# Kernel tuning notes

Measured on AMD Instinct MI355X. Metric: run time of the kernel, lower is better.

## Reference

```python
import jax, jax.numpy as jnp
import numpy as np

N = 8192      # total nodes
B = 8         # graphs in batch
L = 1024      # nodes per graph (max_len)
E = 262144    # edges (before self loops)
IN = 64       # in_channels
H = 8         # heads
C = 32        # hidden_channels (per-head out dim)
D = H * C     # 256, d_model
DFF = 2048    # transformer FFN dim (torch default)
NEG = -1e9


def setup_inputs() -> dict:
    key = jax.random.key(0)
    ks = jax.random.split(key, 24)
    def p(i, shape):
        return jax.random.normal(ks[i], shape, jnp.float32) * 0.02
    x = jax.random.normal(ks[0], (N, IN), jnp.float32)
    src = jax.random.randint(ks[1], (E,), 0, N)
    dst = (src // L) * L + jax.random.randint(ks[2], (E,), 0, L)  # keep edges within a graph
    edge_index = jnp.stack([src, dst]).astype(jnp.int32)
    batch = (jnp.arange(N) // L).astype(jnp.int32)
    return dict(
        x=x, edge_index=edge_index, batch=batch,
        gat_W0=p(3, (D, IN)), gat_W12=p(4, (2, D, D)),
        gat_att_src=p(5, (3, H, C)), gat_att_dst=p(6, (3, H, C)), gat_bias=p(7, (3, D)),
        tf_qkv_w=p(8, (2, 3 * D, D)), tf_qkv_b=p(9, (2, 3 * D)),
        tf_out_w=p(10, (2, D, D)), tf_out_b=p(11, (2, D)),
        tf_ln1_w=jnp.ones((2, D)), tf_ln1_b=jnp.zeros((2, D)),
        tf_ln2_w=jnp.ones((2, D)), tf_ln2_b=jnp.zeros((2, D)),
        tf_ff1_w=p(12, (2, DFF, D)), tf_ff1_b=p(13, (2, DFF)),
        tf_ff2_w=p(14, (2, D, DFF)), tf_ff2_b=p(15, (2, D)),
        pred_w=p(16, (3, D)), pred_b=p(17, (3,)),
    )


def _gat(x, src, dst, W, att_s, att_d, bias):
    # PyG GATConv, concat=True, add_self_loops (appended in caller), eval (no dropout)
    h = (x @ W.T).reshape(-1, H, C)                       # [N,H,C]
    a_s = (h * att_s).sum(-1)                             # [N,H]
    a_d = (h * att_d).sum(-1)
    e = jax.nn.leaky_relu(a_s[src] + a_d[dst], 0.2)       # [E+N,H]
    m = jax.ops.segment_max(e, dst, num_segments=N)       # per-dst softmax
    e = jnp.exp(e - m[dst])
    s = jax.ops.segment_sum(e, dst, num_segments=N)
    alpha = e / s[dst]
    out = jax.ops.segment_sum(h[src] * alpha[..., None], dst, num_segments=N)
    return out.reshape(-1, D) + bias


def _ln(x, w, b):
    mu = x.mean(-1, keepdims=True)
    v = ((x - mu) ** 2).mean(-1, keepdims=True)
    return (x - mu) / jnp.sqrt(v + 1e-5) * w + b


def _tf_layer(x, mask, qkv_w, qkv_b, out_w, out_b, ln1w, ln1b, ln2w, ln2b, f1w, f1b, f2w, f2b):
    # torch TransformerEncoderLayer (post-LN, relu), key padding mask, eval mode
    qkv = x @ qkv_w.T + qkv_b                              # [B,L,3D]
    q, k, v = jnp.split(qkv, 3, -1)
    sh = lambda t: t.reshape(B, L, H, D // H)
    q, k, v = sh(q), sh(k), sh(v)
    sc = jnp.einsum('bqhd,bkhd->bhqk', q, k) * (1.0 / float(np.sqrt(D // H)))
    sc = jnp.where(mask[:, None, None, :], NEG, sc)
    a = jax.nn.softmax(sc, -1)
    o = jnp.einsum('bhqk,bkhd->bqhd', a, v).reshape(B, L, D)
    x = _ln(x + o @ out_w.T + out_b, ln1w, ln1b)
    f = jax.nn.relu(x @ f1w.T + f1b) @ f2w.T + f2b
    return _ln(x + f, ln2w, ln2b)


def reference(x, edge_index, batch, gat_W0, gat_W12, gat_att_src, gat_att_dst, gat_bias,
              tf_qkv_w, tf_qkv_b, tf_out_w, tf_out_b, tf_ln1_w, tf_ln1_b, tf_ln2_w, tf_ln2_b,
              tf_ff1_w, tf_ff1_b, tf_ff2_w, tf_ff2_b, pred_w, pred_b):
    loops = jnp.arange(N, dtype=edge_index.dtype)
    src = jnp.concatenate([edge_index[0], loops])
    dst = jnp.concatenate([edge_index[1], loops])
    h = jax.nn.relu(_gat(x, src, dst, gat_W0, gat_att_src[0], gat_att_dst[0], gat_bias[0]))
    for i in range(2):
        h = jax.nn.relu(_gat(h, src, dst, gat_W12[i], gat_att_src[i + 1], gat_att_dst[i + 1], gat_bias[i + 1]))
    # ragged -> padded [B, L, D] (vectorized scatter instead of python loop)
    seq_lens = jax.ops.segment_sum(jnp.ones(N, jnp.int32), batch, num_segments=B)
    starts = jnp.cumsum(seq_lens) - seq_lens
    pos = jnp.arange(N) - starts[batch]
    xp = jnp.zeros((B, L, D), h.dtype).at[batch, pos].set(h)
    mask = jnp.arange(L)[None, :] >= seq_lens[:, None]     # True = padded key
    for i in range(2):
        xp = _tf_layer(xp, mask, tf_qkv_w[i], tf_qkv_b[i], tf_out_w[i], tf_out_b[i],
                       tf_ln1_w[i], tf_ln1_b[i], tf_ln2_w[i], tf_ln2_b[i],
                       tf_ff1_w[i], tf_ff1_b[i], tf_ff2_w[i], tf_ff2_b[i])
    return xp @ pred_w.T + pred_b                          # [B,L,3]
```

## Files before the change

kernel.cpp:

```cpp
#include <hip/hip_runtime.h>
#include <hip/hip_bf16.h>

#define NN 8192
#define EE 262144
#define BB 8
#define LL 1024
#define HH 8
#define DD 256
#define DFFN 2048

typedef short s8v __attribute__((ext_vector_type(8)));
typedef float f32x4 __attribute__((ext_vector_type(4)));
typedef unsigned short ushort;

__device__ inline ushort f2bf(float f) {
    unsigned u = __float_as_uint(f);
    u = (u + 0x7fffu + ((u >> 16) & 1u)) >> 16;
    return (ushort)u;
}
__device__ inline float bf2f(ushort u) {
    return __uint_as_float(((unsigned)u) << 16);
}

template<bool BIAS, bool RELU, bool RES, bool WF, bool WB>
__global__ __launch_bounds__(256) void mgemm_kernel(
    const ushort* __restrict__ A, const ushort* __restrict__ W,
    const float* __restrict__ bias, const float* __restrict__ res,
    float* __restrict__ Cf, ushort* __restrict__ Cb, int M, int N, int K)
{
    __shared__ ushort As[128 * 64];
    __shared__ ushort Bs[128 * 64];
    int t = threadIdx.x;
    int l = t & 63;
    int quad = l >> 4, l15 = l & 15;
    int r7 = l15 & 7;
    int w = t >> 6;
    int wm = (w >> 1) * 64, wn = (w & 1) * 64;
    int m0 = blockIdx.x * 128, n0 = blockIdx.y * 128;

    f32x4 z = {0.f, 0.f, 0.f, 0.f};
    f32x4 acc[4][4];
#pragma unroll
    for (int i = 0; i < 4; ++i)
#pragma unroll
        for (int j = 0; j < 4; ++j) acc[i][j] = z;

    for (int k0 = 0; k0 < K; k0 += 64) {
#pragma unroll
        for (int i = 0; i < 4; ++i) {
            int chunk = i * 256 + t;
            int r = chunk >> 3, p = chunk & 7;
            int qs = (p ^ (r & 7)) * 8;
            __builtin_amdgcn_global_load_lds(
                (const __attribute__((address_space(1))) unsigned int*)
                    (A + (size_t)(m0 + r) * K + k0 + qs),
                (__attribute__((address_space(3))) unsigned int*)(As + chunk * 8), 16, 0, 0);
            __builtin_amdgcn_global_load_lds(
                (const __attribute__((address_space(1))) unsigned int*)
                    (W + (size_t)(n0 + r) * K + k0 + qs),
                (__attribute__((address_space(3))) unsigned int*)(Bs + chunk * 8), 16, 0, 0);
        }
        __syncthreads();
#pragma unroll
        for (int kk = 0; kk < 2; ++kk) {
            int off = ((kk * 4 + quad) ^ r7) * 8;
            s8v af[4], bfv[4];
#pragma unroll
            for (int i = 0; i < 4; ++i) {
                af[i]  = *(const s8v*)(As + (wm + i * 16 + l15) * 64 + off);
                bfv[i] = *(const s8v*)(Bs + (wn + i * 16 + l15) * 64 + off);
            }
#pragma unroll
            for (int mi = 0; mi < 4; ++mi)
#pragma unroll
                for (int ni = 0; ni < 4; ++ni)
                    acc[mi][ni] = __builtin_amdgcn_mfma_f32_16x16x32_bf16(
                        af[mi], bfv[ni], acc[mi][ni], 0, 0, 0);
        }
        __syncthreads();
    }

#pragma unroll
    for (int mi = 0; mi < 4; ++mi) {
#pragma unroll
        for (int ni = 0; ni < 4; ++ni) {
            int n = n0 + wn + ni * 16 + l15;
#pragma unroll
            for (int r = 0; r < 4; ++r) {
                int m = m0 + wm + mi * 16 + quad * 4 + r;
                float v = acc[mi][ni][r];
                if (BIAS) v += bias[n];
                if (RES)  v += res[(size_t)m * N + n];
                if (RELU) v = fmaxf(v, 0.f);
                if (WF) Cf[(size_t)m * N + n] = v;
                if (WB) Cb[(size_t)m * N + n] = f2bf(v);
            }
        }
    }
}

template<bool BIAS, bool RELU, bool RES, bool WF, bool WB, bool ASD>
__global__ __launch_bounds__(256) void mgemm64_kernel(
    const ushort* __restrict__ A, const ushort* __restrict__ W,
    const float* __restrict__ bias, const float* __restrict__ res,
    float* __restrict__ Cf, ushort* __restrict__ Cb,
    const float* __restrict__ atts, const float* __restrict__ attd,
    float* __restrict__ a_s, float* __restrict__ a_d, int M, int N, int K)
{
    __shared__ ushort As[64 * 64];
    __shared__ ushort Bs[64 * 64];
    int t = threadIdx.x;
    int l = t & 63;
    int quad = l >> 4, l15 = l & 15;
    int r7 = l15 & 7;
    int w = t >> 6;
    int wm = (w >> 1) * 32, wn = (w & 1) * 32;
    int m0 = blockIdx.x * 64, n0 = blockIdx.y * 64;

    f32x4 z = {0.f, 0.f, 0.f, 0.f};
    f32x4 acc[2][2];
#pragma unroll
    for (int i = 0; i < 2; ++i)
#pragma unroll
        for (int j = 0; j < 2; ++j) acc[i][j] = z;

    for (int k0 = 0; k0 < K; k0 += 64) {
#pragma unroll
        for (int i = 0; i < 2; ++i) {
            int chunk = i * 256 + t;
            int r = chunk >> 3, p = chunk & 7;
            int qs = (p ^ (r & 7)) * 8;
            __builtin_amdgcn_global_load_lds(
                (const __attribute__((address_space(1))) unsigned int*)
                    (A + (size_t)(m0 + r) * K + k0 + qs),
                (__attribute__((address_space(3))) unsigned int*)(As + chunk * 8), 16, 0, 0);
            __builtin_amdgcn_global_load_lds(
                (const __attribute__((address_space(1))) unsigned int*)
                    (W + (size_t)(n0 + r) * K + k0 + qs),
                (__attribute__((address_space(3))) unsigned int*)(Bs + chunk * 8), 16, 0, 0);
        }
        __syncthreads();
#pragma unroll
        for (int kk = 0; kk < 2; ++kk) {
            s8v af[2], bfv[2];
            int off = ((kk * 4 + quad) ^ r7) * 8;
#pragma unroll
            for (int i = 0; i < 2; ++i) {
                af[i]  = *(const s8v*)(As + (wm + i * 16 + l15) * 64 + off);
                bfv[i] = *(const s8v*)(Bs + (wn + i * 16 + l15) * 64 + off);
            }
#pragma unroll
            for (int mi = 0; mi < 2; ++mi)
#pragma unroll
                for (int ni = 0; ni < 2; ++ni)
                    acc[mi][ni] = __builtin_amdgcn_mfma_f32_16x16x32_bf16(
                        af[mi], bfv[ni], acc[mi][ni], 0, 0, 0);
        }
        __syncthreads();
    }

#pragma unroll
    for (int mi = 0; mi < 2; ++mi) {
#pragma unroll
        for (int ni = 0; ni < 2; ++ni) {
            int n = n0 + wn + ni * 16 + l15;
#pragma unroll
            for (int r = 0; r < 4; ++r) {
                int m = m0 + wm + mi * 16 + quad * 4 + r;
                float v = acc[mi][ni][r];
                if (BIAS) v += bias[n];
                if (RES)  v += res[(size_t)m * N + n];
                if (RELU) v = fmaxf(v, 0.f);
                if (WF) Cf[(size_t)m * N + n] = v;
                if (WB) Cb[(size_t)m * N + n] = f2bf(v);
            }
        }
    }

    if (ASD) {
        int head = ((n0 + wn) >> 5) & 7;
        float as0 = atts[head * 32 + l15];
        float as1 = atts[head * 32 + 16 + l15];
        float ad0 = attd[head * 32 + l15];
        float ad1 = attd[head * 32 + 16 + l15];
#pragma unroll
        for (int mi = 0; mi < 2; ++mi)
#pragma unroll
            for (int r = 0; r < 4; ++r) {
                float sp = acc[mi][0][r] * as0 + acc[mi][1][r] * as1;
                float dp = acc[mi][0][r] * ad0 + acc[mi][1][r] * ad1;
#pragma unroll
                for (int off = 1; off < 16; off <<= 1) {
                    sp += __shfl_xor(sp, off);
                    dp += __shfl_xor(dp, off);
                }
                if (l15 == 0) {
                    int m = m0 + wm + mi * 16 + quad * 4 + r;
                    a_s[m * 8 + head] = sp;
                    a_d[m * 8 + head] = dp;
                }
            }
    }
}

__global__ __launch_bounds__(256) void mgemm_ln_kernel(
    const ushort* __restrict__ A, const ushort* __restrict__ W,
    const float* __restrict__ bias, const float* __restrict__ res,
    const float* __restrict__ lnw, const float* __restrict__ lnbb,
    float* __restrict__ Xf, ushort* __restrict__ Xb, int M, int K)
{
    __shared__ ushort As[16 * 64];
    __shared__ ushort Bs[256 * 64];
    __shared__ float red[2][4][16];

    int t = threadIdx.x;
    int l = t & 63;
    int quad = l >> 4, l15 = l & 15;
    int r7 = l15 & 7;
    int w = t >> 6;
    int m0 = blockIdx.x * 16;
    int n0w = w * 64;

    f32x4 z = {0.f, 0.f, 0.f, 0.f};
    f32x4 acc[4];
#pragma unroll
    for (int i = 0; i < 4; ++i) acc[i] = z;

    for (int k0 = 0; k0 < K; k0 += 64) {
#pragma unroll
        for (int i = 0; i < 8; ++i) {
            int chunk = i * 256 + t;
            int r = chunk >> 3, p = chunk & 7;
            int qs = (p ^ (r & 7)) * 8;
            __builtin_amdgcn_global_load_lds(
                (const __attribute__((address_space(1))) unsigned int*)
                    (W + (size_t)r * K + k0 + qs),
                (__attribute__((address_space(3))) unsigned int*)(Bs + chunk * 8), 16, 0, 0);
        }
        if (t < 128) {
            int r = t >> 3, p = t & 7;
            int qs = (p ^ (r & 7)) * 8;
            __builtin_amdgcn_global_load_lds(
                (const __attribute__((address_space(1))) unsigned int*)
                    (A + (size_t)(m0 + r) * K + k0 + qs),
                (__attribute__((address_space(3))) unsigned int*)(As + t * 8), 16, 0, 0);
        }
        __syncthreads();
#pragma unroll
        for (int kk = 0; kk < 2; ++kk) {
            int off = ((kk * 4 + quad) ^ r7) * 8;
            s8v af = *(const s8v*)(As + l15 * 64 + off);
#pragma unroll
            for (int ni = 0; ni < 4; ++ni) {
                s8v bfv = *(const s8v*)(Bs + (n0w + ni * 16 + l15) * 64 + off);
                acc[ni] = __builtin_amdgcn_mfma_f32_16x16x32_bf16(af, bfv, acc[ni], 0, 0, 0);
            }
        }
        __syncthreads();
    }

    float v[4][4];
#pragma unroll
    for (int ni = 0; ni < 4; ++ni) {
        int n = n0w + ni * 16 + l15;
        float bi = bias[n];
#pragma unroll
        for (int r = 0; r < 4; ++r) {
            int m = m0 + quad * 4 + r;
            v[ni][r] = acc[ni][r] + bi + res[(size_t)m * DD + n];
        }
    }
    float s1[4], s2[4];
#pragma unroll
    for (int r = 0; r < 4; ++r) {
        s1[r] = 0.f; s2[r] = 0.f;
#pragma unroll
        for (int ni = 0; ni < 4; ++ni) { s1[r] += v[ni][r]; s2[r] += v[ni][r] * v[ni][r]; }
#pragma unroll
        for (int off = 1; off < 16; off <<= 1) {
            s1[r] += __shfl_xor(s1[r], off);
            s2[r] += __shfl_xor(s2[r], off);
        }
    }
    if (l15 == 0)
#pragma unroll
        for (int r = 0; r < 4; ++r) {
            red[0][w][quad * 4 + r] = s1[r];
            red[1][w][quad * 4 + r] = s2[r];
        }
    __syncthreads();
    float mu[4], rstd[4];
#pragma unroll
    for (int r = 0; r < 4; ++r) {
        int row = quad * 4 + r;
        float S1 = red[0][0][row] + red[0][1][row] + red[0][2][row] + red[0][3][row];
        float S2 = red[1][0][row] + red[1][1][row] + red[1][2][row] + red[1][3][row];
        mu[r] = S1 * (1.f / 256.f);
        float var = S2 * (1.f / 256.f) - mu[r] * mu[r];
        rstd[r] = rsqrtf(fmaxf(var, 0.f) + 1e-5f);
    }
#pragma unroll
    for (int ni = 0; ni < 4; ++ni) {
        int n = n0w + ni * 16 + l15;
        float wl = lnw[n], bl = lnbb[n];
#pragma unroll
        for (int r = 0; r < 4; ++r) {
            int m = m0 + quad * 4 + r;
            float o = (v[ni][r] - mu[r]) * rstd[r] * wl + bl;
            Xf[(size_t)m * DD + n] = o;
            Xb[(size_t)m * DD + n] = f2bf(o);
        }
    }
}

__global__ __launch_bounds__(256) void mgemm_qkv_kernel(
    const ushort* __restrict__ A, const ushort* __restrict__ W,
    const float* __restrict__ bias,
    ushort* __restrict__ Qb, ushort* __restrict__ Kb, ushort* __restrict__ Vt,
    int M, int K)
{
    __shared__ ushort As[64 * 64];
    __shared__ ushort Bs[64 * 64];
    int t = threadIdx.x;
    int l = t & 63;
    int quad = l >> 4, l15 = l & 15;
    int r7 = l15 & 7;
    int w = t >> 6;
    int wm = (w >> 1) * 32, wn = (w & 1) * 32;
    int m0 = blockIdx.x * 64, n0 = blockIdx.y * 64;

    f32x4 z = {0.f, 0.f, 0.f, 0.f};
    f32x4 acc[2][2];
#pragma unroll
    for (int i = 0; i < 2; ++i)
#pragma unroll
        for (int j = 0; j < 2; ++j) acc[i][j] = z;

    for (int k0 = 0; k0 < K; k0 += 64) {
#pragma unroll
        for (int i = 0; i < 2; ++i) {
            int chunk = i * 256 + t;
            int r = chunk >> 3, p = chunk & 7;
            int qs = (p ^ (r & 7)) * 8;
            __builtin_amdgcn_global_load_lds(
                (const __attribute__((address_space(1))) unsigned int*)
                    (A + (size_t)(m0 + r) * K + k0 + qs),
                (__attribute__((address_space(3))) unsigned int*)(As + chunk * 8), 16, 0, 0);
            __builtin_amdgcn_global_load_lds(
                (const __attribute__((address_space(1))) unsigned int*)
                    (W + (size_t)(n0 + r) * K + k0 + qs),
                (__attribute__((address_space(3))) unsigned int*)(Bs + chunk * 8), 16, 0, 0);
        }
        __syncthreads();
#pragma unroll
        for (int kk = 0; kk < 2; ++kk) {
            s8v af[2], bfv[2];
            int off = ((kk * 4 + quad) ^ r7) * 8;
#pragma unroll
            for (int i = 0; i < 2; ++i) {
                af[i]  = *(const s8v*)(As + (wm + i * 16 + l15) * 64 + off);
                bfv[i] = *(const s8v*)(Bs + (wn + i * 16 + l15) * 64 + off);
            }
#pragma unroll
            for (int mi = 0; mi < 2; ++mi)
#pragma unroll
                for (int ni = 0; ni < 2; ++ni)
                    acc[mi][ni] = __builtin_amdgcn_mfma_f32_16x16x32_bf16(
                        af[mi], bfv[ni], acc[mi][ni], 0, 0, 0);
        }
        __syncthreads();
    }

#pragma unroll
    for (int mi = 0; mi < 2; ++mi) {
#pragma unroll
        for (int ni = 0; ni < 2; ++ni) {
            int n = n0 + wn + ni * 16 + l15;
            int sec = n >> 8, hc = n & 255;
            int hh = hc >> 5, c = hc & 31;
            float bv = bias[n];
#pragma unroll
            for (int r = 0; r < 4; ++r) {
                int m = m0 + wm + mi * 16 + quad * 4 + r;
                float v = acc[mi][ni][r] + bv;
                int b = m >> 10, ll2 = m & 1023;
                int bh = b * 8 + hh;
                if (sec == 0)
                    Qb[(size_t)bh * 32768 + ll2 * 32 + c] = f2bf(v * 0.17677669529663687f);
                else if (sec == 1)
                    Kb[(size_t)bh * 32768 + ll2 * 32 + c] = f2bf(v);
                else
                    Vt[(size_t)bh * 32768 + c * 1024 + ll2] = f2bf(v);
            }
        }
    }
}

__global__ __launch_bounds__(256) void castall_kernel(
    const float* __restrict__ W0, const float* __restrict__ W12,
    const float* __restrict__ qkvw, const float* __restrict__ outw,
    const float* __restrict__ f1w, const float* __restrict__ f2w,
    const float* __restrict__ x,
    ushort* __restrict__ W0b, ushort* __restrict__ W12b,
    ushort* __restrict__ qkvb, ushort* __restrict__ outb,
    ushort* __restrict__ f1b, ushort* __restrict__ f2b,
    ushort* __restrict__ xb, int* __restrict__ deg)
{
    int tid = blockIdx.x * 256 + threadIdx.x;
    if (tid < 2048) *(int4*)(deg + tid * 4) = make_int4(0, 0, 0, 0);
    int e = tid * 4;
    if (e >= 3293184) return;
    const float* s; ushort* d; int off;
    if (e < 16384)        { s = W0;   d = W0b;  off = e; }
    else if (e < 147456)  { s = W12;  d = W12b; off = e - 16384; }
    else if (e < 540672)  { s = qkvw; d = qkvb; off = e - 147456; }
    else if (e < 671744)  { s = outw; d = outb; off = e - 540672; }
    else if (e < 1720320) { s = f1w;  d = f1b;  off = e - 671744; }
    else if (e < 2768896) { s = f2w;  d = f2b;  off = e - 1720320; }
    else                  { s = x;    d = xb;   off = e - 2768896; }
    float4 v = *(const float4*)(s + off);
    d[off + 0] = f2bf(v.x); d[off + 1] = f2bf(v.y);
    d[off + 2] = f2bf(v.z); d[off + 3] = f2bf(v.w);
}

__global__ void scatter_kernel(const int* __restrict__ ei, int* __restrict__ deg,
                               int* __restrict__ col)
{
    int e = blockIdx.x * 256 + threadIdx.x;
    if (e >= EE + NN) return;
    int s, d;
    if (e < EE) { s = ei[e]; d = ei[EE + e]; } else { s = e - EE; d = s; }
    int slot = atomicAdd(&deg[d], 1);
    col[(d << 7) + slot] = s;
}

__global__ __launch_bounds__(256) void gat_agg_kernel(
    const ushort* __restrict__ hlinb, const float* __restrict__ a_s,
    const float* __restrict__ a_d, const int* __restrict__ deg,
    const int* __restrict__ col, const float* __restrict__ bias,
    float* __restrict__ alpha_e,
    float* __restrict__ out, ushort* __restrict__ outb)
{
    int wid = threadIdx.x >> 6, lane = threadIdx.x & 63;
    int dst = blockIdx.x * 4 + wid;
    int start = dst << 7;
    int end = start + deg[dst];
    float ad[HH];
#pragma unroll
    for (int h = 0; h < HH; ++h) ad[h] = a_d[(size_t)dst * HH + h];

    float sm[HH];
#pragma unroll
    for (int h = 0; h < HH; ++h) sm[h] = 0.f;
    for (int e = start + lane; e < end; e += 64) {
        int s = col[e];
        float* al = alpha_e + (size_t)e * HH;
#pragma unroll
        for (int h = 0; h < HH; ++h) {
            float v = a_s[(size_t)s * HH + h] + ad[h];
            v = v > 0.f ? v : 0.2f * v;
            float p = __expf(v);
            sm[h] += p;
            al[h] = p;
        }
    }
#pragma unroll
    for (int h = 0; h < HH; ++h)
#pragma unroll
        for (int off = 32; off; off >>= 1) sm[h] += __shfl_xor(sm[h], off);

    int myh = lane >> 3;
    float invs = 1.f / sm[myh];
    float a0 = 0.f, a1 = 0.f, a2 = 0.f, a3 = 0.f;
    int e = start;
    for (; e + 4 <= end; e += 4) {
        int s0 = col[e], s1 = col[e + 1], s2 = col[e + 2], s3 = col[e + 3];
        float al0 = alpha_e[(size_t)e * HH + myh] * invs;
        float al1 = alpha_e[(size_t)(e + 1) * HH + myh] * invs;
        float al2 = alpha_e[(size_t)(e + 2) * HH + myh] * invs;
        float al3 = alpha_e[(size_t)(e + 3) * HH + myh] * invs;
        uint2 h0 = *(const uint2*)(hlinb + (size_t)s0 * DD + lane * 4);
        uint2 h1 = *(const uint2*)(hlinb + (size_t)s1 * DD + lane * 4);
        uint2 h2 = *(const uint2*)(hlinb + (size_t)s2 * DD + lane * 4);
        uint2 h3 = *(const uint2*)(hlinb + (size_t)s3 * DD + lane * 4);
        a0 += al0 * bf2f((ushort)(h0.x & 0xffff)) + al1 * bf2f((ushort)(h1.x & 0xffff))
            + al2 * bf2f((ushort)(h2.x & 0xffff)) + al3 * bf2f((ushort)(h3.x & 0xffff));
        a1 += al0 * bf2f((ushort)(h0.x >> 16)) + al1 * bf2f((ushort)(h1.x >> 16))
            + al2 * bf2f((ushort)(h2.x >> 16)) + al3 * bf2f((ushort)(h3.x >> 16));
        a2 += al0 * bf2f((ushort)(h0.y & 0xffff)) + al1 * bf2f((ushort)(h1.y & 0xffff))
            + al2 * bf2f((ushort)(h2.y & 0xffff)) + al3 * bf2f((ushort)(h3.y & 0xffff));
        a3 += al0 * bf2f((ushort)(h0.y >> 16)) + al1 * bf2f((ushort)(h1.y >> 16))
            + al2 * bf2f((ushort)(h2.y >> 16)) + al3 * bf2f((ushort)(h3.y >> 16));
    }
    for (; e < end; ++e) {
        int s = col[e];
        float alpha = alpha_e[(size_t)e * HH + myh] * invs;
        uint2 hv = *(const uint2*)(hlinb + (size_t)s * DD + lane * 4);
        a0 += alpha * bf2f((ushort)(hv.x & 0xffff));
        a1 += alpha * bf2f((ushort)(hv.x >> 16));
        a2 += alpha * bf2f((ushort)(hv.y & 0xffff));
        a3 += alpha * bf2f((ushort)(hv.y >> 16));
    }
    float4 bv = *(const float4*)(bias + lane * 4);
    float r0 = fmaxf(a0 + bv.x, 0.f);
    float r1 = fmaxf(a1 + bv.y, 0.f);
    float r2 = fmaxf(a2 + bv.z, 0.f);
    float r3 = fmaxf(a3 + bv.w, 0.f);
    float* op = out + (size_t)dst * DD + lane * 4;
    op[0] = r0; op[1] = r1; op[2] = r2; op[3] = r3;
    ushort* ob = outb + (size_t)dst * DD + lane * 4;
    ob[0] = f2bf(r0); ob[1] = f2bf(r1); ob[2] = f2bf(r2); ob[3] = f2bf(r3);
}

__global__ __launch_bounds__(256, 2) void attn_flash_kernel(
    const ushort* __restrict__ Qb, const ushort* __restrict__ Kb,
    const ushort* __restrict__ Vt, ushort* __restrict__ outb)
{
    __shared__ ushort Ks[2][128 * 32];
    __shared__ ushort Vs[2][32 * 128];
    __shared__ ushort pw[4][32][132];

    int t = threadIdx.x;
    int w = t >> 6, lane = t & 63;
    int quad = lane >> 4, l15 = lane & 15;
    int kq = (quad ^ ((l15 >> 1) & 3)) * 8;
    int bh = blockIdx.y;
    int q0 = blockIdx.x * 128 + w * 32;
    int b = bh >> 3, h = bh & 7;

    const ushort* qbase = Qb + (size_t)bh * 32768;
    const ushort* kbase = Kb + (size_t)bh * 32768;
    const ushort* vbase = Vt + (size_t)bh * 32768;

    s8v aq0 = *(const s8v*)(qbase + (q0 + l15) * 32 + quad * 8);
    s8v aq1 = *(const s8v*)(qbase + (q0 + 16 + l15) * 32 + quad * 8);

    int i0 = t, i1 = 256 + t;
    int kr0 = i0 >> 2, kcs0 = (((i0 & 3)) ^ ((kr0 >> 1) & 3)) * 8;
    int kr1 = i1 >> 2, kcs1 = (((i1 & 3)) ^ ((kr1 >> 1) & 3)) * 8;
    int vr0 = i0 >> 4, vcs0 = ((i0 & 15) ^ (vr0 & 15)) * 8;
    int vr1 = i1 >> 4, vcs1 = ((i1 & 15) ^ (vr1 & 15)) * 8;

#define STAGE(ch, bf)                                                          \
    {                                                                          \
        int j0 = (ch) * 128;                                                   \
        __builtin_amdgcn_global_load_lds(                                      \
            (const __attribute__((address_space(1))) unsigned int*)            \
                (kbase + (size_t)(j0 + kr0) * 32 + kcs0),                      \
            (__attribute__((address_space(3))) unsigned int*)(Ks[bf] + i0 * 8), 16, 0, 0); \
        __builtin_amdgcn_global_load_lds(                                      \
            (const __attribute__((address_space(1))) unsigned int*)            \
                (kbase + (size_t)(j0 + kr1) * 32 + kcs1),                      \
            (__attribute__((address_space(3))) unsigned int*)(Ks[bf] + i1 * 8), 16, 0, 0); \
        __builtin_amdgcn_global_load_lds(                                      \
            (const __attribute__((address_space(1))) unsigned int*)            \
                (vbase + (size_t)vr0 * 1024 + j0 + vcs0),                      \
            (__attribute__((address_space(3))) unsigned int*)(Vs[bf] + i0 * 8), 16, 0, 0); \
        __builtin_amdgcn_global_load_lds(                                      \
            (const __attribute__((address_space(1))) unsigned int*)            \
                (vbase + (size_t)vr1 * 1024 + j0 + vcs1),                      \
            (__attribute__((address_space(3))) unsigned int*)(Vs[bf] + i1 * 8), 16, 0, 0); \
    }

    f32x4 z = {0.f, 0.f, 0.f, 0.f};
    f32x4 o00 = z, o01 = z, o10 = z, o11 = z;
    float lden0[4] = {0.f, 0.f, 0.f, 0.f};
    float lden1[4] = {0.f, 0.f, 0.f, 0.f};

    STAGE(0, 0);
    for (int ch = 0; ch < 8; ++ch) {
        int bf = ch & 1;
        __syncthreads();
        if (ch < 7) STAGE(ch + 1, bf ^ 1);

        f32x4 s0[8], s1[8];
#pragma unroll
        for (int kk = 0; kk < 8; ++kk) {
            s8v bk = *(const s8v*)(Ks[bf] + (kk * 16 + l15) * 32 + kq);
            s0[kk] = __builtin_amdgcn_mfma_f32_16x16x32_bf16(aq0, bk, z, 0, 0, 0);
            s1[kk] = __builtin_amdgcn_mfma_f32_16x16x32_bf16(aq1, bk, z, 0, 0, 0);
        }

        float cs0[4] = {0.f, 0.f, 0.f, 0.f};
        float cs1[4] = {0.f, 0.f, 0.f, 0.f};
#pragma unroll
        for (int kk = 0; kk < 8; ++kk) {
#pragma unroll
            for (int r = 0; r < 4; ++r) {
                float p0 = __expf(s0[kk][r]);
                float p1 = __expf(s1[kk][r]);
                cs0[r] += p0;
                cs1[r] += p1;
                pw[w][quad * 4 + r][kk * 16 + l15]      = f2bf(p0);
                pw[w][16 + quad * 4 + r][kk * 16 + l15] = f2bf(p1);
            }
        }
#pragma unroll
        for (int r = 0; r < 4; ++r) {
#pragma unroll
            for (int off = 1; off < 16; off <<= 1) {
                cs0[r] += __shfl_xor(cs0[r], off);
                cs1[r] += __shfl_xor(cs1[r], off);
            }
            lden0[r] += cs0[r];
            lden1[r] += cs1[r];
        }

#pragma unroll
        for (int kk = 0; kk < 4; ++kk) {
            s8v ap0 = *(const s8v*)(&pw[w][l15][kk * 32 + quad * 8]);
            s8v ap1 = *(const s8v*)(&pw[w][16 + l15][kk * 32 + quad * 8]);
            int c0 = ((kk * 4 + quad) ^ l15) * 8;
            s8v b0 = *(const s8v*)(Vs[bf] + (size_t)l15 * 128 + c0);
            s8v b1 = *(const s8v*)(Vs[bf] + (size_t)(16 + l15) * 128 + c0);
            o00 = __builtin_amdgcn_mfma_f32_16x16x32_bf16(ap0, b0, o00, 0, 0, 0);
            o01 = __builtin_amdgcn_mfma_f32_16x16x32_bf16(ap0, b1, o01, 0, 0, 0);
            o10 = __builtin_amdgcn_mfma_f32_16x16x32_bf16(ap1, b0, o10, 0, 0, 0);
            o11 = __builtin_amdgcn_mfma_f32_16x16x32_bf16(ap1, b1, o11, 0, 0, 0);
        }
    }
#undef STAGE

#pragma unroll
    for (int r = 0; r < 4; ++r) {
        int row0 = q0 + quad * 4 + r;
        int row1 = row0 + 16;
        float i0v = 1.f / lden0[r];
        float i1v = 1.f / lden1[r];
        outb[(size_t)(b * 1024 + row0) * 256 + h * 32 + l15]      = f2bf(o00[r] * i0v);
        outb[(size_t)(b * 1024 + row0) * 256 + h * 32 + 16 + l15] = f2bf(o01[r] * i0v);
        outb[(size_t)(b * 1024 + row1) * 256 + h * 32 + l15]      = f2bf(o10[r] * i1v);
        outb[(size_t)(b * 1024 + row1) * 256 + h * 32 + 16 + l15] = f2bf(o11[r] * i1v);
    }
}

__global__ __launch_bounds__(256) void ln_kernel(
    float* __restrict__ x, const float* __restrict__ w, const float* __restrict__ b,
    ushort* __restrict__ xb)
{
    int wid = threadIdx.x >> 6, lane = threadIdx.x & 63;
    size_t row = blockIdx.x * 4 + wid;
    float4 v = *(float4*)(x + row * DD + lane * 4);
    float s = v.x + v.y + v.z + v.w;
#pragma unroll
    for (int off = 32; off; off >>= 1) s += __shfl_xor(s, off);
    float mu = s * (1.f / 256.f);
    float dx = v.x - mu, dy = v.y - mu, dz = v.z - mu, dw = v.w - mu;
    float q = dx * dx + dy * dy + dz * dz + dw * dw;
#pragma unroll
    for (int off = 32; off; off >>= 1) q += __shfl_xor(q, off);
    float rstd = rsqrtf(q * (1.f / 256.f) + 1e-5f);
    int c = lane * 4;
    float4 wv = *(const float4*)(w + c);
    float4 bv = *(const float4*)(b + c);
    float4 o;
    o.x = dx * rstd * wv.x + bv.x;
    o.y = dy * rstd * wv.y + bv.y;
    o.z = dz * rstd * wv.z + bv.z;
    o.w = dw * rstd * wv.w + bv.w;
    *(float4*)(x + row * DD + c) = o;
    ushort* ob = xb + row * DD + c;
    ob[0] = f2bf(o.x); ob[1] = f2bf(o.y); ob[2] = f2bf(o.z); ob[3] = f2bf(o.w);
}

__global__ __launch_bounds__(256) void ln_pred_kernel(
    const float* __restrict__ x, const float* __restrict__ w, const float* __restrict__ b,
    const float* __restrict__ pw, const float* __restrict__ pb,
    float* __restrict__ out)
{
    int wid = threadIdx.x >> 6, lane = threadIdx.x & 63;
    size_t row = blockIdx.x * 4 + wid;
    float4 v = *(const float4*)(x + row * DD + lane * 4);
    float s = v.x + v.y + v.z + v.w;
#pragma unroll
    for (int off = 32; off; off >>= 1) s += __shfl_xor(s, off);
    float mu = s * (1.f / 256.f);
    float dx = v.x - mu, dy = v.y - mu, dz = v.z - mu, dw = v.w - mu;
    float q = dx * dx + dy * dy + dz * dz + dw * dw;
#pragma unroll
    for (int off = 32; off; off >>= 1) q += __shfl_xor(q, off);
    float rstd = rsqrtf(q * (1.f / 256.f) + 1e-5f);
    int c = lane * 4;
    float4 wv = *(const float4*)(w + c);
    float4 bv = *(const float4*)(b + c);
    float4 o;
    o.x = dx * rstd * wv.x + bv.x;
    o.y = dy * rstd * wv.y + bv.y;
    o.z = dz * rstd * wv.z + bv.z;
    o.w = dw * rstd * wv.w + bv.w;
    float4 w0 = *(const float4*)(pw + c);
    float4 w1 = *(const float4*)(pw + DD + c);
    float4 w2 = *(const float4*)(pw + 2 * DD + c);
    float s0 = o.x * w0.x + o.y * w0.y + o.z * w0.z + o.w * w0.w;
    float s1 = o.x * w1.x + o.y * w1.y + o.z * w1.z + o.w * w1.w;
    float s2 = o.x * w2.x + o.y * w2.y + o.z * w2.z + o.w * w2.w;
#pragma unroll
    for (int off = 32; off; off >>= 1) {
        s0 += __shfl_xor(s0, off);
        s1 += __shfl_xor(s1, off);
        s2 += __shfl_xor(s2, off);
    }
    if (lane == 0) {
        out[row * 3 + 0] = s0 + pb[0];
        out[row * 3 + 1] = s1 + pb[1];
        out[row * 3 + 2] = s2 + pb[2];
    }
}

extern "C" void kernel_launch(void* const* d_in, const int* in_sizes, int n_in,
                              void* d_out, int out_size, void* d_ws, size_t ws_size,
                              hipStream_t stream)
{
    const float* x        = (const float*)d_in[0];
    const int*   ei       = (const int*)d_in[1];
    const float* gat_W0   = (const float*)d_in[3];
    const float* gat_W12  = (const float*)d_in[4];
    const float* att_src  = (const float*)d_in[5];
    const float* att_dst  = (const float*)d_in[6];
    const float* gat_bias = (const float*)d_in[7];
    const float* qkv_w    = (const float*)d_in[8];
    const float* qkv_b    = (const float*)d_in[9];
    const float* out_w    = (const float*)d_in[10];
    const float* out_b    = (const float*)d_in[11];
    const float* ln1_w    = (const float*)d_in[12];
    const float* ln1_b    = (const float*)d_in[13];
    const float* ln2_w    = (const float*)d_in[14];
    const float* ln2_b    = (const float*)d_in[15];
    const float* ff1_w    = (const float*)d_in[16];
    const float* ff1_b    = (const float*)d_in[17];
    const float* ff2_w    = (const float*)d_in[18];
    const float* ff2_b    = (const float*)d_in[19];
    const float* pred_w   = (const float*)d_in[20];
    const float* pred_b   = (const float*)d_in[21];
    float* outp = (float*)d_out;

    float* ws   = (float*)d_ws;
    float* hA   = ws;
    float* hB   = ws + 2097152;
    ushort* ffb  = (ushort*)(ws + 4194304);
    ushort* Qb   = (ushort*)(ws + 12582912);
    ushort* Kb   = (ushort*)(ws + 13631488);
    ushort* Vt   = (ushort*)(ws + 14680064);
    ushort* attnb= (ushort*)(ws + 15728640);
    ushort* lnb  = (ushort*)(ws + 16777216);
    ushort* hBb  = (ushort*)(ws + 17825792);
    ushort* xb   = (ushort*)(ws + 18874368);
    ushort* wbase= (ushort*)(ws + 19136512);
    ushort* W0b    = wbase;
    ushort* W12b   = wbase + 16384;
    ushort* qkv_wb = wbase + 147456;
    ushort* out_wb = wbase + 540672;
    ushort* ff1_wb = wbase + 671744;
    ushort* ff2_wb = wbase + 1720320;
    float* a_s  = ws + 20520960;
    float* a_d  = ws + 20586496;
    int*   deg  = (int*)(ws + 20652032);
    ushort* hAb    = (ushort*)(ws + 21000192);
    float*  alpha_e = ws + 22048768;
    int*   col  = (int*)(ws + 30437376);

    castall_kernel<<<3216, 256, 0, stream>>>(
        gat_W0, gat_W12, qkv_w, out_w, ff1_w, ff2_w, x,
        W0b, W12b, qkv_wb, out_wb, ff1_wb, ff2_wb, xb, deg);

    scatter_kernel<<<(EE + NN + 255) / 256, 256, 0, stream>>>(ei, deg, col);

    mgemm64_kernel<false, false, false, false, true, true><<<dim3(128, 4), 256, 0, stream>>>(
        xb, W0b, nullptr, nullptr, nullptr, hAb, att_src, att_dst, a_s, a_d, NN, DD, 64);
    gat_agg_kernel<<<2048, 256, 0, stream>>>(hAb, a_s, a_d, deg, col, gat_bias,
                                             alpha_e, hB, hBb);

    for (int l = 0; l < 2; ++l) {
        mgemm64_kernel<false, false, false, false, true, true><<<dim3(128, 4), 256, 0, stream>>>(
            hBb, W12b + (size_t)l * DD * DD, nullptr, nullptr, nullptr, hAb,
            att_src + (l + 1) * 256, att_dst + (l + 1) * 256, a_s, a_d, NN, DD, DD);
        gat_agg_kernel<<<2048, 256, 0, stream>>>(
            hAb, a_s, a_d, deg, col, gat_bias + (l + 1) * 256, alpha_e, hB, hBb);
    }

    for (int l = 0; l < 2; ++l) {
        mgemm_qkv_kernel<<<dim3(128, 12), 256, 0, stream>>>(
            hBb, qkv_wb + (size_t)l * 768 * DD, qkv_b + l * 768, Qb, Kb, Vt, NN, DD);
        attn_flash_kernel<<<dim3(8, 64), 256, 0, stream>>>(Qb, Kb, Vt, attnb);
        mgemm_ln_kernel<<<512, 256, 0, stream>>>(
            attnb, out_wb + (size_t)l * DD * DD, out_b + l * DD, hB,
            ln1_w + l * DD, ln1_b + l * DD, hA, lnb, NN, DD);
        mgemm_kernel<true, true, false, false, true><<<dim3(64, 16), 256, 0, stream>>>(
            lnb, ff1_wb + (size_t)l * DFFN * DD, ff1_b + l * DFFN, nullptr,
            nullptr, ffb, NN, DFFN, DD);
        mgemm64_kernel<true, false, true, true, false, false><<<dim3(128, 4), 256, 0, stream>>>(
            ffb, ff2_wb + (size_t)l * DD * DFFN, ff2_b + l * DD, hA,
            hB, nullptr, nullptr, nullptr, nullptr, nullptr, NN, DD, DFFN);
        if (l == 0) {
            ln_kernel<<<2048, 256, 0, stream>>>(hB, ln2_w + l * DD, ln2_b + l * DD, hBb);
        } else {
            ln_pred_kernel<<<2048, 256, 0, stream>>>(
                hB, ln2_w + l * DD, ln2_b + l * DD, pred_w, pred_b, outp);
        }
    }
}
```

Measured before the change: 394.5 us.

## Fuse FF2 GEMM with LayerNorm/pred head and merge scatter into first GAT GEMM

The FF2 projection now runs through the row-block GEMM+LayerNorm kernel, so the standalone LN and LN+pred kernels are gone and the fp32 FF2 output no longer round-trips through memory. A PRED variant also folds the final 3-way prediction head into that epilogue. The edge scatter is merged into the first GAT GEMM launch as extra blocks, removing one launch and letting both run at once. The tradeoff is that FF2 now uses 16-row tiles over K=2048 with fewer blocks (512) than the previous 64x64 tiling, which may lower GEMM efficiency.

Measured after the change: 393.8 us. Within noise of the previous version (-0.2%).

```diff
diff --git a/kernel.cpp b/kernel.cpp
--- a/kernel.cpp
+++ b/kernel.cpp
@@ -99,11 +99,10 @@
     }
 }
 
-template<bool BIAS, bool RELU, bool RES, bool WF, bool WB, bool ASD>
+template<bool ASD>
 __global__ __launch_bounds__(256) void mgemm64_kernel(
     const ushort* __restrict__ A, const ushort* __restrict__ W,
-    const float* __restrict__ bias, const float* __restrict__ res,
-    float* __restrict__ Cf, ushort* __restrict__ Cb,
+    ushort* __restrict__ Cb,
     const float* __restrict__ atts, const float* __restrict__ attd,
     float* __restrict__ a_s, float* __restrict__ a_d, int M, int N, int K)
 {
@@ -167,12 +166,7 @@
 #pragma unroll
             for (int r = 0; r < 4; ++r) {
                 int m = m0 + wm + mi * 16 + quad * 4 + r;
-                float v = acc[mi][ni][r];
-                if (BIAS) v += bias[n];
-                if (RES)  v += res[(size_t)m * N + n];
-                if (RELU) v = fmaxf(v, 0.f);
-                if (WF) Cf[(size_t)m * N + n] = v;
-                if (WB) Cb[(size_t)m * N + n] = f2bf(v);
+                Cb[(size_t)m * N + n] = f2bf(acc[mi][ni][r]);
             }
         }
     }
@@ -203,15 +197,127 @@
     }
 }
 
+__global__ __launch_bounds__(256) void gemm0_scatter_kernel(
+    const ushort* __restrict__ A, const ushort* __restrict__ W,
+    ushort* __restrict__ Cb,
+    const float* __restrict__ atts, const float* __restrict__ attd,
+    float* __restrict__ a_s, float* __restrict__ a_d,
+    const int* __restrict__ ei, int* __restrict__ deg, int* __restrict__ col)
+{
+    __shared__ ushort As[64 * 64];
+    __shared__ ushort Bs[64 * 64];
+    int t = threadIdx.x;
+
+    if (blockIdx.x >= 512) {
+        int e = (blockIdx.x - 512) * 256 + t;
+        if (e < EE + NN) {
+            int s, d;
+            if (e < EE) { s = ei[e]; d = ei[EE + e]; } else { s = e - EE; d = s; }
+            int slot = atomicAdd(&deg[d], 1);
+            col[(d << 7) + slot] = s;
+        }
+        return;
+    }
+
+    int l = t & 63;
+    int quad = l >> 4, l15 = l & 15;
+    int r7 = l15 & 7;
+    int w = t >> 6;
+    int wm = (w >> 1) * 32, wn = (w & 1) * 32;
+    int m0 = (blockIdx.x & 127) * 64, n0 = (blockIdx.x >> 7) * 64;
+    const int K = 64;
+
+    f32x4 z = {0.f, 0.f, 0.f, 0.f};
+    f32x4 acc[2][2];
+#pragma unroll
+    for (int i = 0; i < 2; ++i)
+#pragma unroll
+        for (int j = 0; j < 2; ++j) acc[i][j] = z;
+
+#pragma unroll
+    for (int i = 0; i < 2; ++i) {
+        int chunk = i * 256 + t;
+        int r = chunk >> 3, p = chunk & 7;
+        int qs = (p ^ (r & 7)) * 8;
+        __builtin_amdgcn_global_load_lds(
+            (const __attribute__((address_space(1))) unsigned int*)
+                (A + (size_t)(m0 + r) * K + qs),
+            (__attribute__((address_space(3))) unsigned int*)(As + chunk * 8), 16, 0, 0);
+        __builtin_amdgcn_global_load_lds(
+            (const __attribute__((address_space(1))) unsigned int*)
+                (W + (size_t)(n0 + r) * K + qs),
+            (__attribute__((address_space(3))) unsigned int*)(Bs + chunk * 8), 16, 0, 0);
+    }
+    __syncthreads();
+#pragma unroll
+    for (int kk = 0; kk < 2; ++kk) {
+        s8v af[2], bfv[2];
+        int off = ((kk * 4 + quad) ^ r7) * 8;
+#pragma unroll
+        for (int i = 0; i < 2; ++i) {
+            af[i]  = *(const s8v*)(As + (wm + i * 16 + l15) * 64 + off);
+            bfv[i] = *(const s8v*)(Bs + (wn + i * 16 + l15) * 64 + off);
+        }
+#pragma unroll
+        for (int mi = 0; mi < 2; ++mi)
+#pragma unroll
+            for (int ni = 0; ni < 2; ++ni)
+                acc[mi][ni] = __builtin_amdgcn_mfma_f32_16x16x32_bf16(
+                    af[mi], bfv[ni], acc[mi][ni], 0, 0, 0);
+    }
+
+#pragma unroll
+    for (int mi = 0; mi < 2; ++mi) {
+#pragma unroll
+        for (int ni = 0; ni < 2; ++ni) {
+            int n = n0 + wn + ni * 16 + l15;
+#pragma unroll
+            for (int r = 0; r < 4; ++r) {
+                int m = m0 + wm + mi * 16 + quad * 4 + r;
+                Cb[(size_t)m * DD + n] = f2bf(acc[mi][ni][r]);
+            }
+        }
+    }
+
+    {
+        int head = ((n0 + wn) >> 5) & 7;
+        float as0 = atts[head * 32 + l15];
+        float as1 = atts[head * 32 + 16 + l15];
+        float ad0 = attd[head * 32 + l15];
+        float ad1 = attd[head * 32 + 16 + l15];
+#pragma unroll
+        for (int mi = 0; mi < 2; ++mi)
+#pragma unroll
+            for (int r = 0; r < 4; ++r) {
+                float sp = acc[mi][0][r] * as0 + acc[mi][1][r] * as1;
+                float dp = acc[mi][0][r] * ad0 + acc[mi][1][r] * ad1;
+#pragma unroll
+                for (int off = 1; off < 16; off <<= 1) {
+                    sp += __shfl_xor(sp, off);
+                    dp += __shfl_xor(dp, off);
+                }
+                if (l15 == 0) {
+                    int m = m0 + wm + mi * 16 + quad * 4 + r;
+                    a_s[m * 8 + head] = sp;
+                    a_d[m * 8 + head] = dp;
+                }
+            }
+    }
+}
+
+template<bool PRED>
 __global__ __launch_bounds__(256) void mgemm_ln_kernel(
     const ushort* __restrict__ A, const ushort* __restrict__ W,
     const float* __restrict__ bias, const float* __restrict__ res,
     const float* __restrict__ lnw, const float* __restrict__ lnbb,
-    float* __restrict__ Xf, ushort* __restrict__ Xb, int M, int K)
+    float* __restrict__ Xf, ushort* __restrict__ Xb,
+    const float* __restrict__ pw, const float* __restrict__ pb,
+    float* __restrict__ pout, int M, int K)
 {
     __shared__ ushort As[16 * 64];
     __shared__ ushort Bs[256 * 64];
     __shared__ float red[2][4][16];
+    __shared__ float predred[4][16][3];
 
     int t = threadIdx.x;
     int l = t & 63;
@@ -299,16 +405,60 @@
         float var = S2 * (1.f / 256.f) - mu[r] * mu[r];
         rstd[r] = rsqrtf(fmaxf(var, 0.f) + 1e-5f);
     }
+
+    float ov[4][4];
 #pragma unroll
     for (int ni = 0; ni < 4; ++ni) {
         int n = n0w + ni * 16 + l15;
         float wl = lnw[n], bl = lnbb[n];
 #pragma unroll
-        for (int r = 0; r < 4; ++r) {
-            int m = m0 + quad * 4 + r;
-            float o = (v[ni][r] - mu[r]) * rstd[r] * wl + bl;
-            Xf[(size_t)m * DD + n] = o;
-            Xb[(size_t)m * DD + n] = f2bf(o);
+        for (int r = 0; r < 4; ++r)
+            ov[ni][r] = (v[ni][r] - mu[r]) * rstd[r] * wl + bl;
+    }
+
+    if (PRED) {
+        float ps[3][4] = {};
+#pragma unroll
+        for (int ni = 0; ni < 4; ++ni) {
+            int n = n0w + ni * 16 + l15;
+            float w0 = pw[n], w1 = pw[DD + n], w2 = pw[2 * DD + n];
+#pragma unroll
+            for (int r = 0; r < 4; ++r) {
+                ps[0][r] += ov[ni][r] * w0;
+                ps[1][r] += ov[ni][r] * w1;
+                ps[2][r] += ov[ni][r] * w2;
+            }
+        }
+#pragma unroll
+        for (int o3 = 0; o3 < 3; ++o3)
+#pragma unroll
+            for (int r = 0; r < 4; ++r)
+#pragma unroll
+                for (int off = 1; off < 16; off <<= 1)
+                    ps[o3][r] += __shfl_xor(ps[o3][r], off);
+        if (l15 == 0)
+#pragma unroll
+            for (int o3 = 0; o3 < 3; ++o3)
+#pragma unroll
+                for (int r = 0; r < 4; ++r)
+                    predred[w][quad * 4 + r][o3] = ps[o3][r];
+        __syncthreads();
+        if (t < 48) {
+            int row = t / 3, o3 = t % 3;
+            float s = predred[0][row][o3] + predred[1][row][o3]
+                    + predred[2][row][o3] + predred[3][row][o3] + pb[o3];
+            pout[(size_t)(m0 + row) * 3 + o3] = s;
+        }
+    } else {
+#pragma unroll
+        for (int ni = 0; ni < 4; ++ni) {
+            int n = n0w + ni * 16 + l15;
+#pragma unroll
+            for (int r = 0; r < 4; ++r) {
+                int m = m0 + quad * 4 + r;
+                Xf[(size_t)m * DD + n] = ov[ni][r];
+                Xb[(size_t)m * DD + n] = f2bf(ov[ni][r]);
+            }
         }
     }
 }
@@ -423,17 +573,6 @@
     d[off + 2] = f2bf(v.z); d[off + 3] = f2bf(v.w);
 }
 
-__global__ void scatter_kernel(const int* __restrict__ ei, int* __restrict__ deg,
-                               int* __restrict__ col)
-{
-    int e = blockIdx.x * 256 + threadIdx.x;
-    if (e >= EE + NN) return;
-    int s, d;
-    if (e < EE) { s = ei[e]; d = ei[EE + e]; } else { s = e - EE; d = s; }
-    int slot = atomicAdd(&deg[d], 1);
-    col[(d << 7) + slot] = s;
-}
-
 __global__ __launch_bounds__(256) void gat_agg_kernel(
     const ushort* __restrict__ hlinb, const float* __restrict__ a_s,
     const float* __restrict__ a_d, const int* __restrict__ deg,
@@ -631,79 +770,6 @@
         outb[(size_t)(b * 1024 + row0) * 256 + h * 32 + 16 + l15] = f2bf(o01[r] * i0v);
         outb[(size_t)(b * 1024 + row1) * 256 + h * 32 + l15]      = f2bf(o10[r] * i1v);
         outb[(size_t)(b * 1024 + row1) * 256 + h * 32 + 16 + l15] = f2bf(o11[r] * i1v);
-    }
-}
-
-__global__ __launch_bounds__(256) void ln_kernel(
-    float* __restrict__ x, const float* __restrict__ w, const float* __restrict__ b,
-    ushort* __restrict__ xb)
-{
-    int wid = threadIdx.x >> 6, lane = threadIdx.x & 63;
-    size_t row = blockIdx.x * 4 + wid;
-    float4 v = *(float4*)(x + row * DD + lane * 4);
-    float s = v.x + v.y + v.z + v.w;
-#pragma unroll
-    for (int off = 32; off; off >>= 1) s += __shfl_xor(s, off);
-    float mu = s * (1.f / 256.f);
-    float dx = v.x - mu, dy = v.y - mu, dz = v.z - mu, dw = v.w - mu;
-    float q = dx * dx + dy * dy + dz * dz + dw * dw;
-#pragma unroll
-    for (int off = 32; off; off >>= 1) q += __shfl_xor(q, off);
-    float rstd = rsqrtf(q * (1.f / 256.f) + 1e-5f);
-    int c = lane * 4;
-    float4 wv = *(const float4*)(w + c);
-    float4 bv = *(const float4*)(b + c);
-    float4 o;
-    o.x = dx * rstd * wv.x + bv.x;
-    o.y = dy * rstd * wv.y + bv.y;
-    o.z = dz * rstd * wv.z + bv.z;
-    o.w = dw * rstd * wv.w + bv.w;
-    *(float4*)(x + row * DD + c) = o;
-    ushort* ob = xb + row * DD + c;
-    ob[0] = f2bf(o.x); ob[1] = f2bf(o.y); ob[2] = f2bf(o.z); ob[3] = f2bf(o.w);
-}
-
-__global__ __launch_bounds__(256) void ln_pred_kernel(
-    const float* __restrict__ x, const float* __restrict__ w, const float* __restrict__ b,
-    const float* __restrict__ pw, const float* __restrict__ pb,
-    float* __restrict__ out)
-{
-    int wid = threadIdx.x >> 6, lane = threadIdx.x & 63;
-    size_t row = blockIdx.x * 4 + wid;
-    float4 v = *(const float4*)(x + row * DD + lane * 4);
-    float s = v.x + v.y + v.z + v.w;
-#pragma unroll
-    for (int off = 32; off; off >>= 1) s += __shfl_xor(s, off);
-    float mu = s * (1.f / 256.f);
-    float dx = v.x - mu, dy = v.y - mu, dz = v.z - mu, dw = v.w - mu;
-    float q = dx * dx + dy * dy + dz * dz + dw * dw;
-#pragma unroll
-    for (int off = 32; off; off >>= 1) q += __shfl_xor(q, off);
-    float rstd = rsqrtf(q * (1.f / 256.f) + 1e-5f);
-    int c = lane * 4;
-    float4 wv = *(const float4*)(w + c);
-    float4 bv = *(const float4*)(b + c);
-    float4 o;
-    o.x = dx * rstd * wv.x + bv.x;
-    o.y = dy * rstd * wv.y + bv.y;
-    o.z = dz * rstd * wv.z + bv.z;
-    o.w = dw * rstd * wv.w + bv.w;
-    float4 w0 = *(const float4*)(pw + c);
-    float4 w1 = *(const float4*)(pw + DD + c);
-    float4 w2 = *(const float4*)(pw + 2 * DD + c);
-    float s0 = o.x * w0.x + o.y * w0.y + o.z * w0.z + o.w * w0.w;
-    float s1 = o.x * w1.x + o.y * w1.y + o.z * w1.z + o.w * w1.w;
-    float s2 = o.x * w2.x + o.y * w2.y + o.z * w2.z + o.w * w2.w;
-#pragma unroll
-    for (int off = 32; off; off >>= 1) {
-        s0 += __shfl_xor(s0, off);
-        s1 += __shfl_xor(s1, off);
-        s2 += __shfl_xor(s2, off);
-    }
-    if (lane == 0) {
-        out[row * 3 + 0] = s0 + pb[0];
-        out[row * 3 + 1] = s1 + pb[1];
-        out[row * 3 + 2] = s2 + pb[2];
     }
 }
 
@@ -763,16 +829,14 @@
         gat_W0, gat_W12, qkv_w, out_w, ff1_w, ff2_w, x,
         W0b, W12b, qkv_wb, out_wb, ff1_wb, ff2_wb, xb, deg);
 
-    scatter_kernel<<<(EE + NN + 255) / 256, 256, 0, stream>>>(ei, deg, col);
-
-    mgemm64_kernel<false, false, false, false, true, true><<<dim3(128, 4), 256, 0, stream>>>(
-        xb, W0b, nullptr, nullptr, nullptr, hAb, att_src, att_dst, a_s, a_d, NN, DD, 64);
+    gemm0_scatter_kernel<<<1568, 256, 0, stream>>>(
+        xb, W0b, hAb, att_src, att_dst, a_s, a_d, ei, deg, col);
     gat_agg_kernel<<<2048, 256, 0, stream>>>(hAb, a_s, a_d, deg, col, gat_bias,
                                              alpha_e, hB, hBb);
 
     for (int l = 0; l < 2; ++l) {
-        mgemm64_kernel<false, false, false, false, true, true><<<dim3(128, 4), 256, 0, stream>>>(
-            hBb, W12b + (size_t)l * DD * DD, nullptr, nullptr, nullptr, hAb,
+        mgemm64_kernel<true><<<dim3(128, 4), 256, 0, stream>>>(
+            hBb, W12b + (size_t)l * DD * DD, hAb,
             att_src + (l + 1) * 256, att_dst + (l + 1) * 256, a_s, a_d, NN, DD, DD);
         gat_agg_kernel<<<2048, 256, 0, stream>>>(
             hAb, a_s, a_d, deg, col, gat_bias + (l + 1) * 256, alpha_e, hB, hBb);
@@ -782,20 +846,23 @@
         mgemm_qkv_kernel<<<dim3(128, 12), 256, 0, stream>>>(
             hBb, qkv_wb + (size_t)l * 768 * DD, qkv_b + l * 768, Qb, Kb, Vt, NN, DD);
         attn_flash_kernel<<<dim3(8, 64), 256, 0, stream>>>(Qb, Kb, Vt, attnb);
-        mgemm_ln_kernel<<<512, 256, 0, stream>>>(
+        mgemm_ln_kernel<false><<<512, 256, 0, stream>>>(
             attnb, out_wb + (size_t)l * DD * DD, out_b + l * DD, hB,
-            ln1_w + l * DD, ln1_b + l * DD, hA, lnb, NN, DD);
+            ln1_w + l * DD, ln1_b + l * DD, hA, lnb,
+            nullptr, nullptr, nullptr, NN, DD);
         mgemm_kernel<true, true, false, false, true><<<dim3(64, 16), 256, 0, stream>>>(
             lnb, ff1_wb + (size_t)l * DFFN * DD, ff1_b + l * DFFN, nullptr,
             nullptr, ffb, NN, DFFN, DD);
-        mgemm64_kernel<true, false, true, true, false, false><<<dim3(128, 4), 256, 0, stream>>>(
-            ffb, ff2_wb + (size_t)l * DD * DFFN, ff2_b + l * DD, hA,
-            hB, nullptr, nullptr, nullptr, nullptr, nullptr, NN, DD, DFFN);
         if (l == 0) {
-            ln_kernel<<<2048, 256, 0, stream>>>(hB, ln2_w + l * DD, ln2_b + l * DD, hBb);
+            mgemm_ln_kernel<false><<<512, 256, 0, stream>>>(
+                ffb, ff2_wb, ff2_b, hA,
+                ln2_w, ln2_b, hB, hBb,
+                nullptr, nullptr, nullptr, NN, DFFN);
         } else {
-            ln_pred_kernel<<<2048, 256, 0, stream>>>(
-                hB, ln2_w + l * DD, ln2_b + l * DD, pred_w, pred_b, outp);
-        }
-    }
-}
+            mgemm_ln_kernel<true><<<512, 256, 0, stream>>>(
+                ffb, ff2_wb + (size_t)DD * DFFN, ff2_b + DD, hA,
+                ln2_w + DD, ln2_b + DD, nullptr, nullptr,
+                pred_w, pred_b, outp, NN, DFFN);
+        }
+    }
+}
```
